# Kernel optimization log

Hardware: AMD Instinct MI355X
Metric: run time of the kernel (lower is better)

The kernel has to match this reference:

```python
import jax, jax.numpy as jnp
import numpy as np


def table_operator(A, B):
    # A, B: (size, batch). Returns (16, size, batch) of soft logic-gate outputs.
    AB = A * B
    A_or_B = A + B - AB
    A_xor_B = A + B - 2.0 * AB
    return jnp.stack([
        jnp.zeros_like(A),          # 0: FALSE
        AB,                         # 1: A AND B
        A - AB,                     # 2: A AND NOT B
        A,                          # 3: A
        B - AB,                     # 4: NOT A AND B
        B,                          # 5: B
        A_xor_B,                    # 6: A XOR B
        A_or_B,                     # 7: A OR B
        1.0 - A_or_B,               # 8: NOR
        1.0 - A_xor_B,              # 9: XNOR
        1.0 - B,                    # 10: NOT B
        1.0 - B + AB,               # 11: B -> A
        1.0 - A,                    # 12: NOT A
        1.0 - A + AB,               # 13: A -> B
        1.0 - AB,                   # 14: NAND
        jnp.ones_like(A),           # 15: TRUE
    ], axis=0)


def setup_inputs() -> dict:
    key = jax.random.key(0)
    k1, k2, k3, k4 = jax.random.split(key, 4)
    prev_size, size, batch = 1024, 1024, 16384
    return {
        "prev_layer_output": jax.random.uniform(k1, (prev_size, batch), jnp.float32),
        "input_A_weights": jax.random.normal(k2, (size, prev_size), jnp.float32),
        "input_B_weights": jax.random.normal(k3, (size, prev_size), jnp.float32),
        "table_weights": jax.random.normal(k4, (16, size), jnp.float32),
    }


def reference(prev_layer_output, input_A_weights, input_B_weights, table_weights):
    # Inference path (torch.is_grad_enabled() == False, drop_out_rate == 0):
    # plain softmaxes, no multiplier shift, no dropout. GradFactor is identity in fwd.
    pA = jax.nn.softmax(input_A_weights, axis=1)   # (size, prev_size)
    pB = jax.nn.softmax(input_B_weights, axis=1)
    pT = jax.nn.softmax(table_weights, axis=0)     # (16, size)
    a = pA @ prev_layer_output                     # (size, batch)
    b = pB @ prev_layer_output                     # (size, batch)
    gates = table_operator(a, b)                   # (16, size, batch)
    return jnp.sum(gates * pT[:, :, None], axis=0)  # (size, batch)
```

## Files before the change

### kernel.cpp

```cpp
#include <hip/hip_runtime.h>
#include <hip/hip_bf16.h>


typedef __attribute__((ext_vector_type(8))) short bf16x8;
typedef __attribute__((ext_vector_type(4))) float f32x4;

__device__ __forceinline__ void gload_lds16(const void* g, void* l) {
    __builtin_amdgcn_global_load_lds(
        (const __attribute__((address_space(1))) void*)g,
        (__attribute__((address_space(3))) void*)l, 16, 0, 0);
}

__global__ __launch_bounds__(256) void softmax_rows_bf16(
    const float* __restrict__ WA, const float* __restrict__ WB,
    __hip_bfloat16* __restrict__ PA, __hip_bfloat16* __restrict__ PB,
    int rows, int cols)
{
    const int b = blockIdx.x;
    const float* W;
    __hip_bfloat16* P;
    if (b < rows) { W = WA + (size_t)b * cols;          P = PA + (size_t)b * cols; }
    else          { W = WB + (size_t)(b - rows) * cols; P = PB + (size_t)(b - rows) * cols; }

    const int t = threadIdx.x;
    const int wave = t >> 6, lane = t & 63;

    float4 v = *(const float4*)&W[t * 4];
    float mx = fmaxf(fmaxf(v.x, v.y), fmaxf(v.z, v.w));
    #pragma unroll
    for (int off = 32; off; off >>= 1) mx = fmaxf(mx, __shfl_xor(mx, off));

    __shared__ float redmax[4];
    __shared__ float redsum[4];
    if (lane == 0) redmax[wave] = mx;
    __syncthreads();
    mx = fmaxf(fmaxf(redmax[0], redmax[1]), fmaxf(redmax[2], redmax[3]));

    float e0 = __expf(v.x - mx), e1 = __expf(v.y - mx);
    float e2 = __expf(v.z - mx), e3 = __expf(v.w - mx);
    float s = e0 + e1 + e2 + e3;
    #pragma unroll
    for (int off = 32; off; off >>= 1) s += __shfl_xor(s, off);
    if (lane == 0) redsum[wave] = s;
    __syncthreads();
    s = redsum[0] + redsum[1] + redsum[2] + redsum[3];

    const float inv = 1.0f / s;
    __align__(8) __hip_bfloat16 o[4];
    o[0] = __float2bfloat16(e0 * inv);
    o[1] = __float2bfloat16(e1 * inv);
    o[2] = __float2bfloat16(e2 * inv);
    o[3] = __float2bfloat16(e3 * inv);
    *(uint2*)&P[t * 4] = *(const uint2*)o;
}

__global__ void table_coef(const float* __restrict__ TW, float4* __restrict__ coef, int size)
{
    const int s = blockIdx.x * blockDim.x + threadIdx.x;
    if (s >= size) return;
    float p[16];
    float mx = -1e30f;
    #pragma unroll
    for (int g = 0; g < 16; ++g) { p[g] = TW[g * size + s]; mx = fmaxf(mx, p[g]); }
    float sum = 0.f;
    #pragma unroll
    for (int g = 0; g < 16; ++g) { p[g] = __expf(p[g] - mx); sum += p[g]; }
    const float inv = 1.0f / sum;
    #pragma unroll
    for (int g = 0; g < 16; ++g) p[g] *= inv;

    float w0  = p[8] + p[9] + p[10] + p[11] + p[12] + p[13] + p[14] + p[15];
    float wA  = p[2] + p[3] + p[6] + p[7] - p[8] - p[9] - p[12] - p[13];
    float wB  = p[4] + p[5] + p[6] + p[7] - p[8] - p[9] - p[10] - p[11];
    float wAB = p[1] - p[2] - p[4] - 2.f * p[6] - p[7]
              + p[8] + 2.f * p[9] + p[11] + p[13] - p[14];
    coef[s] = make_float4(w0, wA, wB, wAB);
}

__global__ __launch_bounds__(256) void transpose_bf16(
    const float* __restrict__ prev, __hip_bfloat16* __restrict__ prevT,
    int K, int N)
{
    __shared__ float ls[64][65];
    const int k0 = blockIdx.y * 64, n0 = blockIdx.x * 64;
    const int t = threadIdx.x;

    {
        const int kr = t >> 4, nc = (t & 15) * 4;
        #pragma unroll
        for (int i = 0; i < 4; ++i) {
            const int k = i * 16 + kr;
            float4 v = *(const float4*)&prev[(size_t)(k0 + k) * N + n0 + nc];
            ls[k][nc + 0] = v.x; ls[k][nc + 1] = v.y;
            ls[k][nc + 2] = v.z; ls[k][nc + 3] = v.w;
        }
    }
    __syncthreads();
    {
        const int n = t >> 2, kc = (t & 3) * 16;
        __align__(16) __hip_bfloat16 tmp[16];
        #pragma unroll
        for (int j = 0; j < 16; ++j) tmp[j] = __float2bfloat16(ls[kc + j][n]);
        __hip_bfloat16* dst = &prevT[(size_t)(n0 + n) * K + k0 + kc];
        *(uint4*)(dst + 0) = *(const uint4*)&tmp[0];
        *(uint4*)(dst + 8) = *(const uint4*)&tmp[8];
    }
}

constexpr int Kd = 1024;
constexpr int Nd = 16384;

__global__ __launch_bounds__(512, 2) void dual_gemm8(
    const __hip_bfloat16* __restrict__ pA,
    const __hip_bfloat16* __restrict__ pB,
    const __hip_bfloat16* __restrict__ prevT,
    const float4* __restrict__ coef,
    float* __restrict__ out)
{
    __shared__ __align__(16) char smem[131072];

    const int t_ = threadIdx.x;
    const int wave = t_ >> 6, lane = t_ & 63;
    const int wr = wave >> 2, wc = wave & 3;
    const int m0 = blockIdx.y * 128;
    const int n0 = blockIdx.x * 256;

    const int fr  = lane & 15;
    const int kg  = lane >> 4;
    const int fsw = fr & 7;
    const int c0 = (kg ^ fsw) * 16;
    const int c1 = ((4 + kg) ^ fsw) * 16;
    const int aoffs = (wr * 128 + fr) * 128;
    const int boffs = 32768 + (wc * 64 + fr) * 128;

    const int sr  = lane >> 3;
    const int swz = ((lane & 7) ^ sr) * 8;
    const int r0  = wave * 16 + sr;
    const __hip_bfloat16* gA0 = pA    + (size_t)(m0 + r0) * Kd + swz;
    const __hip_bfloat16* gA1 = pB    + (size_t)(m0 + r0) * Kd + swz;
    const __hip_bfloat16* gB0 = prevT + (size_t)(n0 + r0) * Kd + swz;
    const __hip_bfloat16* gB1 = prevT + (size_t)(n0 + 128 + r0) * Kd + swz;

    f32x4 acc[8][4] = {};
    bf16x8 a[8], b[8];

#define STG(GP, BB, HOFF, KT) {                                             \
    char* lb = smem + (BB) + (HOFF) + wave * 2048;                          \
    gload_lds16((GP) + (KT), lb);                                           \
    gload_lds16((GP) + (KT) + 8 * Kd, lb + 1024); }

#define RD_ALO(BB) _Pragma("unroll") for (int i = 0; i < 4; ++i) {          \
    a[i*2]   = *(const bf16x8*)(smem + (BB) + aoffs + i * 2048 + c0);       \
    a[i*2+1] = *(const bf16x8*)(smem + (BB) + aoffs + i * 2048 + c1); }
#define RD_AHI(BB) _Pragma("unroll") for (int i = 0; i < 4; ++i) {          \
    a[i*2]   = *(const bf16x8*)(smem + (BB) + aoffs + 8192 + i * 2048 + c0);\
    a[i*2+1] = *(const bf16x8*)(smem + (BB) + aoffs + 8192 + i * 2048 + c1); }
#define RD_BLO(BB) _Pragma("unroll") for (int j = 0; j < 2; ++j) {          \
    b[j*2]   = *(const bf16x8*)(smem + (BB) + boffs + j * 2048 + c0);       \
    b[j*2+1] = *(const bf16x8*)(smem + (BB) + boffs + j * 2048 + c1); }
#define RD_BHI(BB) _Pragma("unroll") for (int j = 0; j < 2; ++j) {          \
    b[4+j*2]   = *(const bf16x8*)(smem + (BB) + boffs + 4096 + j * 2048 + c0); \
    b[4+j*2+1] = *(const bf16x8*)(smem + (BB) + boffs + 4096 + j * 2048 + c1); }

#define BAR __builtin_amdgcn_s_barrier()
#define VMW(S) asm volatile("s_waitcnt " S ::: "memory")

#define MM(I0, J0, BB0)                                                     \
    asm volatile("s_waitcnt lgkmcnt(0)" ::: "memory");                      \
    __builtin_amdgcn_sched_barrier(0);                                      \
    __builtin_amdgcn_s_setprio(1);                                          \
    _Pragma("unroll") for (int i = 0; i < 4; ++i)                           \
    _Pragma("unroll") for (int j = 0; j < 2; ++j)                           \
    _Pragma("unroll") for (int ks = 0; ks < 2; ++ks)                        \
        acc[(I0)+i][(J0)+j] = __builtin_amdgcn_mfma_f32_16x16x32_bf16(      \
            a[i*2+ks], b[(BB0)+j*2+ks], acc[(I0)+i][(J0)+j], 0, 0, 0);      \
    __builtin_amdgcn_s_setprio(0);

#define TILE(T, CURB, NXTB, SG, SG1, VMSTR) {                               \
    RD_ALO(CURB) RD_BLO(CURB)                                               \
    if (SG) STG(gB1, NXTB, 49152, ((T)+1)*64)                               \
    asm volatile("s_waitcnt lgkmcnt(8)" ::: "memory");                      \
    BAR;                                                                    \
    MM(0, 0, 0) BAR;                                                        \
    RD_BHI(CURB)                                                            \
    if (SG) STG(gA0, NXTB, 0, ((T)+1)*64)                                   \
    BAR;                                                                    \
    MM(0, 2, 4) BAR;                                                        \
    RD_AHI(CURB)                                                            \
    if (SG) STG(gA1, NXTB, 16384, ((T)+1)*64)                               \
    BAR;                                                                    \
    MM(4, 2, 4) BAR;                                                        \
    if (SG1) STG(gB0, CURB, 32768, ((T)+2)*64)                              \
    VMW(VMSTR); BAR;                                                        \
    MM(4, 0, 0) BAR;                                                        \
}

    STG(gB0, 0, 32768, 0)
    STG(gB1, 0, 49152, 0)
    STG(gA0, 0, 0,     0)
    STG(gA1, 0, 16384, 0)
    STG(gB0, 65536, 32768, 64)
    VMW("vmcnt(2)");
    BAR;

    for (int t = 0; t < 14; t += 2) {
        TILE(t,     0,     65536, 1, 1, "vmcnt(2)")
        TILE(t + 1, 65536, 0,     1, 1, "vmcnt(2)")
    }
    TILE(14, 0,     65536, 1, 0, "vmcnt(0)")
    TILE(15, 65536, 0,     0, 0, "vmcnt(0)")

#undef TILE
#undef MM
#undef STG
#undef RD_ALO
#undef RD_AHI
#undef RD_BLO
#undef RD_BHI
#undef BAR
#undef VMW

    __syncthreads();
    if (wr == 1) {
        #pragma unroll
        for (int i = 0; i < 8; ++i) {
            #pragma unroll
            for (int j = 0; j < 4; ++j) {
                const int off = ((((wc * 8 + i) * 4 + j) * 64) + lane) * 16;
                *(f32x4*)(smem + off) = acc[i][j];
            }
        }
    }
    __syncthreads();
    if (wr == 0) {
        const int hi = lane >> 4;
        #pragma unroll
        for (int i = 0; i < 8; ++i) {
            float4 cc[4];
            #pragma unroll
            for (int r = 0; r < 4; ++r) cc[r] = coef[m0 + i * 16 + hi * 4 + r];
            #pragma unroll
            for (int j = 0; j < 4; ++j) {
                const f32x4 bb = *(const f32x4*)(smem + ((((wc * 8 + i) * 4 + j) * 64) + lane) * 16);
                const int n = n0 + wc * 64 + j * 16 + fr;
                #pragma unroll
                for (int r = 0; r < 4; ++r) {
                    const int m = m0 + i * 16 + hi * 4 + r;
                    const float aa = acc[i][j][r];
                    out[(size_t)m * Nd + n] = cc[r].x + cc[r].y * aa + cc[r].z * bb[r]
                                            + cc[r].w * (aa * bb[r]);
                }
            }
        }
    }
}

extern "C" void kernel_launch(void* const* d_in, const int* in_sizes, int n_in,
                              void* d_out, int out_size, void* d_ws, size_t ws_size,
                              hipStream_t stream)
{
    const float* prev = (const float*)d_in[0];
    const float* WA   = (const float*)d_in[1];
    const float* WB   = (const float*)d_in[2];
    const float* TW   = (const float*)d_in[3];
    float* out = (float*)d_out;

    const int size      = in_sizes[3] / 16;
    const int prev_size = in_sizes[1] / size;
    const int batch     = in_sizes[0] / prev_size;

    char* ws = (char*)d_ws;
    __hip_bfloat16* prevT = (__hip_bfloat16*)ws;
    size_t off = (size_t)batch * prev_size * sizeof(__hip_bfloat16);
    __hip_bfloat16* pA = (__hip_bfloat16*)(ws + off);
    off += (size_t)size * prev_size * sizeof(__hip_bfloat16);
    __hip_bfloat16* pB = (__hip_bfloat16*)(ws + off);
    off += (size_t)size * prev_size * sizeof(__hip_bfloat16);
    float4* coef = (float4*)(ws + off);

    softmax_rows_bf16<<<dim3(2 * size), dim3(256), 0, stream>>>(
        WA, WB, pA, pB, size, prev_size);
    table_coef<<<dim3((size + 255) / 256), dim3(256), 0, stream>>>(TW, coef, size);
    transpose_bf16<<<dim3(batch / 64, prev_size / 64), dim3(256), 0, stream>>>(
        prev, prevT, prev_size, batch);
    dual_gemm8<<<dim3(batch / 256, size / 128), dim3(512), 0, stream>>>(
        pA, pB, prevT, coef, out);
}
```

Before: 89.65 us.

## Reschedule GEMM main loop: prefetch both B halves two tiles ahead, drop barriers

Restructures the double-buffered bf16 MFMA main loop. Both B halves are now staged two K-tiles ahead, and the A halves one tile ahead. The LDS reads for the next tile's low A/B fragments move to the end of the current tile. The post-MFMA barriers are removed, cutting the barrier count per tile roughly in half. The aim is to hide global-to-LDS latency and reduce synchronisation stalls, at the risk of LDS read/write races if the reordered barriers and vmcnt waits are not sufficient.

Result: no change. 90.47 us (+0.9%).

```diff
diff --git a/kernel.cpp b/kernel.cpp
--- a/kernel.cpp
+++ b/kernel.cpp
@@ -176,41 +176,44 @@
             a[i*2+ks], b[(BB0)+j*2+ks], acc[(I0)+i][(J0)+j], 0, 0, 0);      \
     __builtin_amdgcn_s_setprio(0);
 
-#define TILE(T, CURB, NXTB, SG, SG1, VMSTR) {                               \
-    RD_ALO(CURB) RD_BLO(CURB)                                               \
-    if (SG) STG(gB1, NXTB, 49152, ((T)+1)*64)                               \
-    asm volatile("s_waitcnt lgkmcnt(8)" ::: "memory");                      \
+#define TILE(T, CURB, NXTB, SGA, SGB2, VM4, DORD) {                         \
+    STG_IF(SGA, gA0, NXTB, 0, ((T)+1)*64)                                   \
     BAR;                                                                    \
-    MM(0, 0, 0) BAR;                                                        \
+    MM(0, 0, 0)                                                             \
     RD_BHI(CURB)                                                            \
-    if (SG) STG(gA0, NXTB, 0, ((T)+1)*64)                                   \
+    STG_IF(SGA, gA1, NXTB, 16384, ((T)+1)*64)                               \
     BAR;                                                                    \
-    MM(0, 2, 4) BAR;                                                        \
+    MM(0, 2, 4)                                                             \
     RD_AHI(CURB)                                                            \
-    if (SG) STG(gA1, NXTB, 16384, ((T)+1)*64)                               \
+    STG_IF(SGB2, gB0, CURB, 32768, ((T)+2)*64)                              \
     BAR;                                                                    \
-    MM(4, 2, 4) BAR;                                                        \
-    if (SG1) STG(gB0, CURB, 32768, ((T)+2)*64)                              \
-    VMW(VMSTR); BAR;                                                        \
-    MM(4, 0, 0) BAR;                                                        \
-}
-
+    MM(4, 2, 4)                                                             \
+    STG_IF(SGB2, gB1, CURB, 49152, ((T)+2)*64)                              \
+    VMW(VM4); BAR;                                                          \
+    MM(4, 0, 0)                                                             \
+    if (DORD) { RD_ALO(NXTB) RD_BLO(NXTB) }                                 \
+}
+#define STG_IF(C, GP, BB, HOFF, KT) if (C) STG(GP, BB, HOFF, KT)
+
+    STG(gA0, 0, 0,     0)
+    STG(gA1, 0, 16384, 0)
     STG(gB0, 0, 32768, 0)
     STG(gB1, 0, 49152, 0)
-    STG(gA0, 0, 0,     0)
-    STG(gA1, 0, 16384, 0)
     STG(gB0, 65536, 32768, 64)
-    VMW("vmcnt(2)");
+    STG(gB1, 65536, 49152, 64)
+    VMW("vmcnt(4)");
     BAR;
+    RD_ALO(0) RD_BLO(0)
 
     for (int t = 0; t < 14; t += 2) {
-        TILE(t,     0,     65536, 1, 1, "vmcnt(2)")
-        TILE(t + 1, 65536, 0,     1, 1, "vmcnt(2)")
-    }
-    TILE(14, 0,     65536, 1, 0, "vmcnt(0)")
-    TILE(15, 65536, 0,     0, 0, "vmcnt(0)")
+        TILE(t,     0,     65536, 1, 1, "vmcnt(4)", 1)
+        TILE(t + 1, 65536, 0,     1, 1, "vmcnt(4)", 1)
+    }
+    TILE(14, 0,     65536, 1, 0, "vmcnt(0)", 1)
+    TILE(15, 65536, 0,     0, 0, "vmcnt(0)", 0)
 
 #undef TILE
+#undef STG_IF
 #undef MM
 #undef STG
 #undef RD_ALO
```

## Restructure GEMM main loop with separate fragment registers and one barrier per tile

Applied to the files above, without the earlier changes.

Splits the A/B fragment registers into low and high halves so LDS reads for the next MFMA quadrant can be issued while the current quadrant computes. The next tile's first fragments are also prefetched before the last quadrant. The many per-quadrant s_barriers and lgkmcnt(0) waits are replaced by sched_barriers plus a single vmcnt(0) and barrier per K tile, and the loop is collapsed to a runtime-indexed double-buffered loop. This trades barrier and LDS-latency stalls for more VGPR pressure and a full vmcnt(0) drain each tile, which serialises global prefetch with compute. It also relies on the compiler inserting the correct lgkmcnt waits for LDS data, which could affect correctness or timing.

New measurement: 90.13 us. Within noise of the previous version (+0.5%).

```diff
diff --git a/kernel.cpp b/kernel.cpp
--- a/kernel.cpp
+++ b/kernel.cpp
@@ -142,82 +142,84 @@
     const __hip_bfloat16* gB1 = prevT + (size_t)(n0 + 128 + r0) * Kd + swz;
 
     f32x4 acc[8][4] = {};
-    bf16x8 a[8], b[8];
+    bf16x8 aL[8], aH[8], bL[4], bH[4];
 
 #define STG(GP, BB, HOFF, KT) {                                             \
     char* lb = smem + (BB) + (HOFF) + wave * 2048;                          \
     gload_lds16((GP) + (KT), lb);                                           \
     gload_lds16((GP) + (KT) + 8 * Kd, lb + 1024); }
 
-#define RD_ALO(BB) _Pragma("unroll") for (int i = 0; i < 4; ++i) {          \
-    a[i*2]   = *(const bf16x8*)(smem + (BB) + aoffs + i * 2048 + c0);       \
-    a[i*2+1] = *(const bf16x8*)(smem + (BB) + aoffs + i * 2048 + c1); }
-#define RD_AHI(BB) _Pragma("unroll") for (int i = 0; i < 4; ++i) {          \
-    a[i*2]   = *(const bf16x8*)(smem + (BB) + aoffs + 8192 + i * 2048 + c0);\
-    a[i*2+1] = *(const bf16x8*)(smem + (BB) + aoffs + 8192 + i * 2048 + c1); }
-#define RD_BLO(BB) _Pragma("unroll") for (int j = 0; j < 2; ++j) {          \
-    b[j*2]   = *(const bf16x8*)(smem + (BB) + boffs + j * 2048 + c0);       \
-    b[j*2+1] = *(const bf16x8*)(smem + (BB) + boffs + j * 2048 + c1); }
-#define RD_BHI(BB) _Pragma("unroll") for (int j = 0; j < 2; ++j) {          \
-    b[4+j*2]   = *(const bf16x8*)(smem + (BB) + boffs + 4096 + j * 2048 + c0); \
-    b[4+j*2+1] = *(const bf16x8*)(smem + (BB) + boffs + 4096 + j * 2048 + c1); }
-
-#define BAR __builtin_amdgcn_s_barrier()
+#define RD_AL(BB) _Pragma("unroll") for (int i = 0; i < 4; ++i) {           \
+    aL[i*2]   = *(const bf16x8*)(smem + (BB) + aoffs + i * 2048 + c0);      \
+    aL[i*2+1] = *(const bf16x8*)(smem + (BB) + aoffs + i * 2048 + c1); }
+#define RD_AH(BB) _Pragma("unroll") for (int i = 0; i < 4; ++i) {           \
+    aH[i*2]   = *(const bf16x8*)(smem + (BB) + aoffs + 8192 + i * 2048 + c0); \
+    aH[i*2+1] = *(const bf16x8*)(smem + (BB) + aoffs + 8192 + i * 2048 + c1); }
+#define RD_BL(BB) _Pragma("unroll") for (int j = 0; j < 2; ++j) {           \
+    bL[j*2]   = *(const bf16x8*)(smem + (BB) + boffs + j * 2048 + c0);      \
+    bL[j*2+1] = *(const bf16x8*)(smem + (BB) + boffs + j * 2048 + c1); }
+#define RD_BH(BB) _Pragma("unroll") for (int j = 0; j < 2; ++j) {           \
+    bH[j*2]   = *(const bf16x8*)(smem + (BB) + boffs + 4096 + j * 2048 + c0); \
+    bH[j*2+1] = *(const bf16x8*)(smem + (BB) + boffs + 4096 + j * 2048 + c1); }
+
+#define SB  __builtin_amdgcn_sched_barrier(0)
 #define VMW(S) asm volatile("s_waitcnt " S ::: "memory")
 
-#define MM(I0, J0, BB0)                                                     \
-    asm volatile("s_waitcnt lgkmcnt(0)" ::: "memory");                      \
-    __builtin_amdgcn_sched_barrier(0);                                      \
+#define MMQ(AB, BB, I0, J0)                                                 \
     __builtin_amdgcn_s_setprio(1);                                          \
     _Pragma("unroll") for (int i = 0; i < 4; ++i)                           \
     _Pragma("unroll") for (int j = 0; j < 2; ++j)                           \
     _Pragma("unroll") for (int ks = 0; ks < 2; ++ks)                        \
         acc[(I0)+i][(J0)+j] = __builtin_amdgcn_mfma_f32_16x16x32_bf16(      \
-            a[i*2+ks], b[(BB0)+j*2+ks], acc[(I0)+i][(J0)+j], 0, 0, 0);      \
+            AB[i*2+ks], BB[j*2+ks], acc[(I0)+i][(J0)+j], 0, 0, 0);          \
     __builtin_amdgcn_s_setprio(0);
 
-#define TILE(T, CURB, NXTB, SG, SG1, VMSTR) {                               \
-    RD_ALO(CURB) RD_BLO(CURB)                                               \
-    if (SG) STG(gB1, NXTB, 49152, ((T)+1)*64)                               \
-    asm volatile("s_waitcnt lgkmcnt(8)" ::: "memory");                      \
-    BAR;                                                                    \
-    MM(0, 0, 0) BAR;                                                        \
-    RD_BHI(CURB)                                                            \
-    if (SG) STG(gA0, NXTB, 0, ((T)+1)*64)                                   \
-    BAR;                                                                    \
-    MM(0, 2, 4) BAR;                                                        \
-    RD_AHI(CURB)                                                            \
-    if (SG) STG(gA1, NXTB, 16384, ((T)+1)*64)                               \
-    BAR;                                                                    \
-    MM(4, 2, 4) BAR;                                                        \
-    if (SG1) STG(gB0, CURB, 32768, ((T)+2)*64)                              \
-    VMW(VMSTR); BAR;                                                        \
-    MM(4, 0, 0) BAR;                                                        \
+#define TILE(T, CURB, NXTB, SG) {                                           \
+    if (SG) { STG(gB0, NXTB, 32768, ((T)+1)*64) }                           \
+    RD_BH(CURB)                                                             \
+    SB;                                                                     \
+    MMQ(aL, bL, 0, 0)                                                       \
+    if (SG) { STG(gB1, NXTB, 49152, ((T)+1)*64) }                           \
+    RD_AH(CURB)                                                             \
+    SB;                                                                     \
+    MMQ(aL, bH, 0, 2)                                                       \
+    if (SG) { STG(gA0, NXTB, 0, ((T)+1)*64)                                 \
+              STG(gA1, NXTB, 16384, ((T)+1)*64) }                           \
+    SB;                                                                     \
+    MMQ(aH, bH, 4, 2)                                                       \
+    VMW("vmcnt(0)");                                                        \
+    __builtin_amdgcn_s_barrier();                                           \
+    SB;                                                                     \
+    if (SG) { RD_AL(NXTB) }                                                 \
+    SB;                                                                     \
+    MMQ(aH, bL, 4, 0)                                                       \
+    if (SG) { RD_BL(NXTB) }                                                 \
+    SB;                                                                     \
 }
 
     STG(gB0, 0, 32768, 0)
     STG(gB1, 0, 49152, 0)
     STG(gA0, 0, 0,     0)
     STG(gA1, 0, 16384, 0)
-    STG(gB0, 65536, 32768, 64)
-    VMW("vmcnt(2)");
-    BAR;
-
-    for (int t = 0; t < 14; t += 2) {
-        TILE(t,     0,     65536, 1, 1, "vmcnt(2)")
-        TILE(t + 1, 65536, 0,     1, 1, "vmcnt(2)")
-    }
-    TILE(14, 0,     65536, 1, 0, "vmcnt(0)")
-    TILE(15, 65536, 0,     0, 0, "vmcnt(0)")
+    VMW("vmcnt(0)");
+    __builtin_amdgcn_s_barrier();
+    SB;
+    RD_AL(0) RD_BL(0)
+
+    for (int t = 0; t < 15; ++t) {
+        const int cb = (t & 1) << 16;
+        TILE(t, cb, cb ^ 65536, 1)
+    }
+    TILE(15, 65536, 0, 0)
 
 #undef TILE
-#undef MM
+#undef MMQ
 #undef STG
-#undef RD_ALO
-#undef RD_AHI
-#undef RD_BLO
-#undef RD_BHI
-#undef BAR
+#undef RD_AL
+#undef RD_AH
+#undef RD_BL
+#undef RD_BH
+#undef SB
 #undef VMW
 
     __syncthreads();
```

## Fuse prev transpose and bf16 conversion into the GEMM's B-tile loading

Applied to the files above, without the earlier changes.

Drops the separate transpose_bf16 kernel. The GEMM now reads fp32 prev directly into registers, converts it to bf16 and writes it transposed and swizzled into LDS. The per-tile pipeline is simplified to one barrier per k-tile with register-staged B loads issued ahead of the MFMAs. This removes a full write and re-read of the 32MB bf16 intermediate and one launch. In exchange, each GEMM block reads fp32 B (twice the bytes, once per M-block row of the grid), with more register pressure and VALU conversion work inside the main loop.

New measurement: 90.81 us. About the same (+1.3%).

```diff
diff --git a/kernel.cpp b/kernel.cpp
--- a/kernel.cpp
+++ b/kernel.cpp
@@ -77,43 +77,13 @@
     coef[s] = make_float4(w0, wA, wB, wAB);
 }
 
-__global__ __launch_bounds__(256) void transpose_bf16(
-    const float* __restrict__ prev, __hip_bfloat16* __restrict__ prevT,
-    int K, int N)
-{
-    __shared__ float ls[64][65];
-    const int k0 = blockIdx.y * 64, n0 = blockIdx.x * 64;
-    const int t = threadIdx.x;
-
-    {
-        const int kr = t >> 4, nc = (t & 15) * 4;
-        #pragma unroll
-        for (int i = 0; i < 4; ++i) {
-            const int k = i * 16 + kr;
-            float4 v = *(const float4*)&prev[(size_t)(k0 + k) * N + n0 + nc];
-            ls[k][nc + 0] = v.x; ls[k][nc + 1] = v.y;
-            ls[k][nc + 2] = v.z; ls[k][nc + 3] = v.w;
-        }
-    }
-    __syncthreads();
-    {
-        const int n = t >> 2, kc = (t & 3) * 16;
-        __align__(16) __hip_bfloat16 tmp[16];
-        #pragma unroll
-        for (int j = 0; j < 16; ++j) tmp[j] = __float2bfloat16(ls[kc + j][n]);
-        __hip_bfloat16* dst = &prevT[(size_t)(n0 + n) * K + k0 + kc];
-        *(uint4*)(dst + 0) = *(const uint4*)&tmp[0];
-        *(uint4*)(dst + 8) = *(const uint4*)&tmp[8];
-    }
-}
-
 constexpr int Kd = 1024;
 constexpr int Nd = 16384;
 
 __global__ __launch_bounds__(512, 2) void dual_gemm8(
     const __hip_bfloat16* __restrict__ pA,
     const __hip_bfloat16* __restrict__ pB,
-    const __hip_bfloat16* __restrict__ prevT,
+    const float* __restrict__ prev,
     const float4* __restrict__ coef,
     float* __restrict__ out)
 {
@@ -136,10 +106,13 @@
     const int sr  = lane >> 3;
     const int swz = ((lane & 7) ^ sr) * 8;
     const int r0  = wave * 16 + sr;
-    const __hip_bfloat16* gA0 = pA    + (size_t)(m0 + r0) * Kd + swz;
-    const __hip_bfloat16* gA1 = pB    + (size_t)(m0 + r0) * Kd + swz;
-    const __hip_bfloat16* gB0 = prevT + (size_t)(n0 + r0) * Kd + swz;
-    const __hip_bfloat16* gB1 = prevT + (size_t)(n0 + 128 + r0) * Kd + swz;
+    const __hip_bfloat16* gA0 = pA + (size_t)(m0 + r0) * Kd + swz;
+    const __hip_bfloat16* gA1 = pB + (size_t)(m0 + r0) * Kd + swz;
+
+    const int bl   = lane & 15;
+    const int bkh  = lane >> 4;
+    const int bnloc = wave * 32 + bl * 2;
+    float2 bst[2][8];
 
     f32x4 acc[8][4] = {};
     bf16x8 a[8], b[8];
@@ -148,6 +121,22 @@
     char* lb = smem + (BB) + (HOFF) + wave * 2048;                          \
     gload_lds16((GP) + (KT), lb);                                           \
     gload_lds16((GP) + (KT) + 8 * Kd, lb + 1024); }
+
+#define LOADB(KT) _Pragma("unroll") for (int cp = 0; cp < 2; ++cp)          \
+    _Pragma("unroll") for (int j = 0; j < 8; ++j)                           \
+        bst[cp][j] = *(const float2*)&prev[                                 \
+            (size_t)((KT) + (bkh * 2 + cp) * 8 + j) * Nd + n0 + bnloc];
+
+#define WRITEB(BB) _Pragma("unroll") for (int cp = 0; cp < 2; ++cp)         \
+    _Pragma("unroll") for (int e = 0; e < 2; ++e) {                         \
+        union { __hip_bfloat16 h[8]; bf16x8 v; } u;                         \
+        _Pragma("unroll") for (int j = 0; j < 8; ++j)                       \
+            u.h[j] = __float2bfloat16(e ? bst[cp][j].y : bst[cp][j].x);     \
+        const int rw = bnloc + e;                                           \
+        const int kc = bkh * 2 + cp;                                        \
+        *(bf16x8*)(smem + (BB) + 32768 + rw * 128 +                         \
+                   ((kc ^ (rw & 7)) << 4)) = u.v;                           \
+    }
 
 #define RD_ALO(BB) _Pragma("unroll") for (int i = 0; i < 4; ++i) {          \
     a[i*2]   = *(const bf16x8*)(smem + (BB) + aoffs + i * 2048 + c0);       \
@@ -162,12 +151,9 @@
     b[4+j*2]   = *(const bf16x8*)(smem + (BB) + boffs + 4096 + j * 2048 + c0); \
     b[4+j*2+1] = *(const bf16x8*)(smem + (BB) + boffs + 4096 + j * 2048 + c1); }
 
-#define BAR __builtin_amdgcn_s_barrier()
 #define VMW(S) asm volatile("s_waitcnt " S ::: "memory")
 
-#define MM(I0, J0, BB0)                                                     \
-    asm volatile("s_waitcnt lgkmcnt(0)" ::: "memory");                      \
-    __builtin_amdgcn_sched_barrier(0);                                      \
+#define MMQ(I0, J0, BB0)                                                    \
     __builtin_amdgcn_s_setprio(1);                                          \
     _Pragma("unroll") for (int i = 0; i < 4; ++i)                           \
     _Pragma("unroll") for (int j = 0; j < 2; ++j)                           \
@@ -176,48 +162,47 @@
             a[i*2+ks], b[(BB0)+j*2+ks], acc[(I0)+i][(J0)+j], 0, 0, 0);      \
     __builtin_amdgcn_s_setprio(0);
 
-#define TILE(T, CURB, NXTB, SG, SG1, VMSTR) {                               \
+#define TILE(T, CURB, NXTB, SG) {                                           \
+    if (SG) { LOADB(((T)+1)*64)                                             \
+              STG(gA0, NXTB, 0, ((T)+1)*64)                                 \
+              STG(gA1, NXTB, 16384, ((T)+1)*64) }                           \
     RD_ALO(CURB) RD_BLO(CURB)                                               \
-    if (SG) STG(gB1, NXTB, 49152, ((T)+1)*64)                               \
-    asm volatile("s_waitcnt lgkmcnt(8)" ::: "memory");                      \
-    BAR;                                                                    \
-    MM(0, 0, 0) BAR;                                                        \
+    MMQ(0, 0, 0)                                                            \
     RD_BHI(CURB)                                                            \
-    if (SG) STG(gA0, NXTB, 0, ((T)+1)*64)                                   \
-    BAR;                                                                    \
-    MM(0, 2, 4) BAR;                                                        \
+    MMQ(0, 2, 4)                                                            \
     RD_AHI(CURB)                                                            \
-    if (SG) STG(gA1, NXTB, 16384, ((T)+1)*64)                               \
-    BAR;                                                                    \
-    MM(4, 2, 4) BAR;                                                        \
-    if (SG1) STG(gB0, CURB, 32768, ((T)+2)*64)                              \
-    VMW(VMSTR); BAR;                                                        \
-    MM(4, 0, 0) BAR;                                                        \
-}
-
-    STG(gB0, 0, 32768, 0)
-    STG(gB1, 0, 49152, 0)
+    MMQ(4, 2, 4)                                                            \
+    MMQ(4, 0, 0)                                                            \
+    if (SG) { VMW("vmcnt(0)"); WRITEB(NXTB) }                               \
+    asm volatile("s_waitcnt lgkmcnt(0)" ::: "memory");                      \
+    __builtin_amdgcn_s_barrier();                                           \
+    __builtin_amdgcn_sched_barrier(0);                                      \
+}
+
+    LOADB(0)
     STG(gA0, 0, 0,     0)
     STG(gA1, 0, 16384, 0)
-    STG(gB0, 65536, 32768, 64)
-    VMW("vmcnt(2)");
-    BAR;
-
-    for (int t = 0; t < 14; t += 2) {
-        TILE(t,     0,     65536, 1, 1, "vmcnt(2)")
-        TILE(t + 1, 65536, 0,     1, 1, "vmcnt(2)")
-    }
-    TILE(14, 0,     65536, 1, 0, "vmcnt(0)")
-    TILE(15, 65536, 0,     0, 0, "vmcnt(0)")
+    VMW("vmcnt(0)");
+    WRITEB(0)
+    asm volatile("s_waitcnt lgkmcnt(0)" ::: "memory");
+    __builtin_amdgcn_s_barrier();
+    __builtin_amdgcn_sched_barrier(0);
+
+    for (int t = 0; t < 15; ++t) {
+        const int cb = (t & 1) << 16;
+        TILE(t, cb, cb ^ 65536, 1)
+    }
+    TILE(15, 65536, 0, 0)
 
 #undef TILE
-#undef MM
+#undef MMQ
 #undef STG
+#undef LOADB
+#undef WRITEB
 #undef RD_ALO
 #undef RD_AHI
 #undef RD_BLO
 #undef RD_BHI
-#undef BAR
 #undef VMW
 
     __syncthreads();
@@ -270,10 +255,8 @@
     const int batch     = in_sizes[0] / prev_size;
 
     char* ws = (char*)d_ws;
-    __hip_bfloat16* prevT = (__hip_bfloat16*)ws;
-    size_t off = (size_t)batch * prev_size * sizeof(__hip_bfloat16);
-    __hip_bfloat16* pA = (__hip_bfloat16*)(ws + off);
-    off += (size_t)size * prev_size * sizeof(__hip_bfloat16);
+    __hip_bfloat16* pA = (__hip_bfloat16*)ws;
+    size_t off = (size_t)size * prev_size * sizeof(__hip_bfloat16);
     __hip_bfloat16* pB = (__hip_bfloat16*)(ws + off);
     off += (size_t)size * prev_size * sizeof(__hip_bfloat16);
     float4* coef = (float4*)(ws + off);
@@ -281,8 +264,6 @@
     softmax_rows_bf16<<<dim3(2 * size), dim3(256), 0, stream>>>(
         WA, WB, pA, pB, size, prev_size);
     table_coef<<<dim3((size + 255) / 256), dim3(256), 0, stream>>>(TW, coef, size);
-    transpose_bf16<<<dim3(batch / 64, prev_size / 64), dim3(256), 0, stream>>>(
-        prev, prevT, prev_size, batch);
     dual_gemm8<<<dim3(batch / 256, size / 128), dim3(512), 0, stream>>>(
-        pA, pB, prevT, coef, out);
-}
+        pA, pB, prev, coef, out);
+}
```
